# Kernel tuning notes

Hardware: AMD Instinct MI355X
Metric: run time of the kernel (lower is better)

Reference implementation:

```python
import jax, jax.numpy as jnp
import numpy as np

V, E, S, B, T = 100000, 64, 4, 2048, 200
D = 2 * E          # memory_vector_dim
C = E              # controller_units
CIN = 2 * E + D    # controller input: x_t (2E) + prev read (D)
P = 2 * (D + 1) + 2 * D  # (key+beta) for read & write heads + erase + add


def setup_inputs() -> dict:
    key = jax.random.key(0)
    ks = jax.random.split(key, 16)
    g = lambda k, sh, sc=0.05: jax.random.normal(k, sh, dtype=jnp.float32) * sc
    return {
        "item": jax.random.randint(ks[0], (B,), 0, V),
        "cate": jax.random.randint(ks[1], (B,), 0, V),
        "hist_item": jax.random.randint(ks[2], (B, T), 0, V),
        "hist_cate": jax.random.randint(ks[3], (B, T), 0, V),
        "mask": jnp.ones((B, T), jnp.float32),
        "embedding": g(ks[4], (V, E)),
        "gru_Wih": g(ks[5], (3 * C, CIN)),
        "gru_Whh": g(ks[6], (3 * C, C)),
        "gru_bih": jnp.zeros((3 * C,), jnp.float32),
        "gru_bhh": jnp.zeros((3 * C,), jnp.float32),
        "Wp": g(ks[7], (P, C)),
        "bp": jnp.zeros((P,), jnp.float32),
        "Wo": g(ks[8], (E, C + D)),
        "bo": jnp.zeros((E,), jnp.float32),
        "M0": g(ks[9], (S, D), 0.1),
        "fc1_w": g(ks[10], (200, 5 * E)),
        "fc1_b": jnp.zeros((200,), jnp.float32),
        "prelu1_a": jnp.full((1,), 0.25, jnp.float32),
        "fc2_w": g(ks[11], (80, 200)),
        "fc2_b": jnp.zeros((80,), jnp.float32),
        "prelu2_a": jnp.full((1,), 0.25, jnp.float32),
        "fc3_w": g(ks[12], (2, 80)),
        "fc3_b": jnp.zeros((2,), jnp.float32),
    }


def _cos_addr(k, beta, M):
    # content addressing: softmax(beta * cosine_sim(k, M))  k:[B,D] M:[B,S,D]
    kn = k / (jnp.linalg.norm(k, axis=-1, keepdims=True) + 1e-8)
    Mn = M / (jnp.linalg.norm(M, axis=-1, keepdims=True) + 1e-8)
    K = jnp.einsum('bd,bsd->bs', kn, Mn)
    return jax.nn.softmax(beta[:, None] * K, axis=-1)


def _prelu(x, a):
    return jnp.where(x > 0, x, a * x)


def _mimn_rnn(hist_emb, mask, gru_Wih, gru_Whh, gru_bih, gru_bhh, Wp, bp, Wo, bo, M0):
    Bn = hist_emb.shape[0]
    h0 = jnp.zeros((Bn, C), hist_emb.dtype)
    r0 = jnp.zeros((Bn, D), hist_emb.dtype)
    Mi = jnp.broadcast_to(M0[None], (Bn, S, D))

    def step(carry, inp):
        h, M, read = carry
        x_t, m_t = inp                      # x_t [B,2E], m_t [B]
        ctrl_in = jnp.concatenate([x_t, read], axis=-1)
        gi = ctrl_in @ gru_Wih.T + gru_bih
        gh = h @ gru_Whh.T + gru_bhh
        i_r, i_z, i_n = jnp.split(gi, 3, axis=-1)
        h_r, h_z, h_n = jnp.split(gh, 3, axis=-1)
        rg = jax.nn.sigmoid(i_r + h_r)
        zg = jax.nn.sigmoid(i_z + h_z)
        ng = jnp.tanh(i_n + rg * h_n)
        h_new = (1.0 - zg) * ng + zg * h
        # head parameters
        p = h_new @ Wp.T + bp               # [B, P]
        hp_r, hp_w = p[:, :D + 1], p[:, D + 1:2 * (D + 1)]
        erase = jax.nn.sigmoid(p[:, 2 * (D + 1):2 * (D + 1) + D])
        add = jnp.tanh(p[:, -D:])
        k_r, beta_r = jnp.tanh(hp_r[:, :D]), jax.nn.softplus(hp_r[:, D])
        k_w, beta_w = jnp.tanh(hp_w[:, :D]), jax.nn.softplus(hp_w[:, D])
        w_r = _cos_addr(k_r, beta_r, M)
        w_w = _cos_addr(k_w, beta_w, M)
        read_new = jnp.einsum('bs,bsd->bd', w_r, M)
        M_new = M * (1.0 - w_w[..., None] * erase[:, None, :]) + w_w[..., None] * add[:, None, :]
        out = jnp.concatenate([h_new, read_new], axis=-1) @ Wo.T + bo  # [B,E]
        # sequence-length masking (dynamic_rnn semantics)
        v = (m_t > 0)[:, None]
        h = jnp.where(v, h_new, h)
        read = jnp.where(v, read_new, read)
        M = jnp.where(v[..., None], M_new, M)
        out = jnp.where(v, out, jnp.zeros_like(out))
        return (h, M, read), out

    xs = (jnp.swapaxes(hist_emb, 0, 1), jnp.swapaxes(mask, 0, 1))  # [T,B,...]
    _, outs = jax.lax.scan(step, (h0, Mi, r0), xs)
    return jnp.swapaxes(outs, 0, 1)  # [B,T,E]


def reference(item, cate, hist_item, hist_cate, mask, embedding,
              gru_Wih, gru_Whh, gru_bih, gru_bhh, Wp, bp, Wo, bo, M0,
              fc1_w, fc1_b, prelu1_a, fc2_w, fc2_b, prelu2_a, fc3_w, fc3_b):
    item_emb = jnp.concatenate([embedding[item], embedding[cate]], axis=1)      # [B,2E]
    hist_emb = jnp.concatenate([embedding[hist_item], embedding[hist_cate]], axis=2)  # [B,T,2E]
    seq_len = mask.sum(1).astype(jnp.int32)
    outputs = _mimn_rnn(hist_emb, mask, gru_Wih, gru_Whh, gru_bih, gru_bhh, Wp, bp, Wo, bo, M0)
    last_out = jnp.take_along_axis(outputs, (seq_len - 1)[:, None, None], axis=1)[:, 0, :]
    hist_sum = (hist_emb * mask[..., None]).sum(1)                              # [B,2E]
    x = jnp.concatenate([item_emb, hist_sum, last_out], axis=1)                 # [B,5E]
    x = _prelu(x @ fc1_w.T + fc1_b, prelu1_a)
    x = _prelu(x @ fc2_w.T + fc2_b, prelu2_a)
    return x @ fc3_w.T + fc3_b
```

## Files before the change

kernel.cpp:

```cpp
#include <hip/hip_runtime.h>

#define VV 100000
#define BB 2048
#define TT 200
#define GG 192
#define PP 514
#define RPB 8

typedef _Float16 half8 __attribute__((ext_vector_type(8)));
typedef float floatx4 __attribute__((ext_vector_type(4)));
#define MFMA16(a, b, c) __builtin_amdgcn_mfma_f32_16x16x32_f16((a), (b), (c), 0, 0, 0)

__device__ __forceinline__ float fsigm(float x) { return 1.0f / (1.0f + __expf(-x)); }
__device__ __forceinline__ float ftanh(float x) {
    float e = __expf(2.0f * x);
    return 1.0f - 2.0f / (e + 1.0f);
}
__device__ __forceinline__ float fsoftplus(float x) {
    float e = __expf(-fabsf(x));
    return fmaxf(x, 0.0f) + __logf(1.0f + e);
}

#define DPP_ADD(x, ctrl, rmask) \
    ((x) + __int_as_float(__builtin_amdgcn_update_dpp( \
        0, __float_as_int(x), (ctrl), (rmask), 0xf, true)))
__device__ __forceinline__ float wsum64(float x) {
    x = DPP_ADD(x, 0x111, 0xf);
    x = DPP_ADD(x, 0x112, 0xf);
    x = DPP_ADD(x, 0x114, 0xf);
    x = DPP_ADD(x, 0x118, 0xf);
    x = DPP_ADD(x, 0x142, 0xa);
    x = DPP_ADD(x, 0x143, 0xc);
    return __int_as_float(__builtin_amdgcn_readlane(__float_as_int(x), 63));
}
__device__ __forceinline__ float dot4(float4 w, float4 a) {
    return w.x * a.x + w.y * a.y + w.z * a.z + w.w * a.w;
}

__global__ __launch_bounds__(192) void build_tables(
    const float* __restrict__ emb,
    const float* __restrict__ Wih,
    const float* __restrict__ bih,
    float* __restrict__ GIi, float* __restrict__ GIc)
{
    __shared__ float sE[64 * 64];
    int tid = threadIdx.x;
    int v0 = blockIdx.x * 64;
    for (int i = tid; i < 64 * 64; i += 192) {
        int vv = i >> 6, k = i & 63;
        int gv = v0 + vv;
        sE[i] = (gv < VV) ? emb[(size_t)gv * 64 + k] : 0.0f;
    }
    __syncthreads();
    int n = tid;
    float bi = bih[n];
    {
        float4 w[16];
        const float4* wp = (const float4*)(Wih + n * 256);
#pragma unroll
        for (int q = 0; q < 16; ++q) w[q] = wp[q];
        for (int vv = 0; vv < 64; ++vv) {
            int gv = v0 + vv;
            if (gv >= VV) break;
            const float4* e = (const float4*)&sE[vv * 64];
            float acc = bi;
#pragma unroll
            for (int q = 0; q < 16; ++q) acc += dot4(w[q], e[q]);
            GIi[(size_t)gv * GG + n] = acc;
        }
    }
    {
        float4 w[16];
        const float4* wp = (const float4*)(Wih + n * 256 + 64);
#pragma unroll
        for (int q = 0; q < 16; ++q) w[q] = wp[q];
        for (int vv = 0; vv < 64; ++vv) {
            int gv = v0 + vv;
            if (gv >= VV) break;
            const float4* e = (const float4*)&sE[vv * 64];
            float acc = 0.0f;
#pragma unroll
            for (int q = 0; q < 16; ++q) acc += dot4(w[q], e[q]);
            GIc[(size_t)gv * GG + n] = acc;
        }
    }
}

__global__ __launch_bounds__(128) void hist_stats(
    const int* __restrict__ hist_item, const int* __restrict__ hist_cate,
    const float* __restrict__ mask, const float* __restrict__ emb,
    float* __restrict__ hist_sum, int* __restrict__ seqlen)
{
    int b = blockIdx.x, tid = threadIdx.x;
    const int* hidx = (tid < 64) ? hist_item : hist_cate;
    int j = tid & 63;
    float acc = 0.f;
    for (int t = 0; t < TT; ++t) {
        float m = mask[b * TT + t];
        int idx = hidx[b * TT + t];
        acc += m * emb[(size_t)idx * 64 + j];
    }
    hist_sum[(size_t)b * 128 + tid] = acc;
    if (tid < 64) {
        float s = 0.f;
        for (int t = tid; t < TT; t += 64) s += mask[b * TT + t];
        s = wsum64(s);
        if (tid == 0) seqlen[b] = (int)(s + 0.5f);
    }
}

__global__ __attribute__((amdgpu_flat_work_group_size(512, 512))) void mimn_rnn(
    const int* __restrict__ hist_item, const int* __restrict__ hist_cate,
    const float* __restrict__ mask,
    const float* __restrict__ Wih,
    const float* __restrict__ Whh,
    const float* __restrict__ bhh,
    const float* __restrict__ Wp,
    const float* __restrict__ bp,
    const float* __restrict__ Wo,
    const float* __restrict__ bo,
    const float* __restrict__ M0,
    const float* __restrict__ GIi, const float* __restrict__ GIc,
    const int* __restrict__ seqlen,
    float* __restrict__ last_out)
{
    __shared__ __align__(16) float sU[4160];
    __shared__ __align__(16) _Float16 act16[16 * 200];
    __shared__ __align__(16) _Float16 hn16[16 * 72];
    __shared__ __align__(16) float sGI2[2 * RPB * 192];
    __shared__ float sHf[RPB * 64];
    __shared__ float sHnF[RPB * 64];
    __shared__ float sM [RPB * 512];
    __shared__ float sBp[PP];
    __shared__ float sBhh[GG];
    __shared__ float sWpT[2 * 64];
    __shared__ unsigned char sMaskB[RPB * TT];

    const int tid = threadIdx.x;
    const int b0 = blockIdx.x * RPB;
    const int wv = tid >> 6, lane = tid & 63;
    const int nlo = lane & 15, kg = lane >> 4;
    const bool hasN = wv >= 4;

    for (int i = tid; i < 16 * 200; i += 512) act16[i] = (_Float16)0.f;
    for (int i = tid; i < 16 * 72; i += 512) hn16[i] = (_Float16)0.f;
    for (int i = tid; i < RPB * 64; i += 512) { sHf[i] = 0.f; sHnF[i] = 0.f; }
    for (int i = tid; i < RPB * 512; i += 512) sM[i] = M0[i & 511];
    for (int i = tid; i < PP; i += 512) sBp[i] = bp[i];
    if (tid < GG) sBhh[tid] = bhh[tid];
    if (tid < 128) sWpT[tid] = Wp[512 * 64 + tid];
    for (int i = tid; i < RPB * TT; i += 512) {
        int r = i / TT, tt = i - r * TT;
        sMaskB[i] = (mask[(size_t)(b0 + r) * TT + tt] > 0.f) ? 1 : 0;
    }

    half8 WG[6];
    {
        int n = 16 * wv + nlo;
#pragma unroll
        for (int kb = 0; kb < 6; ++kb) {
            half8 f;
#pragma unroll
            for (int j = 0; j < 8; ++j) {
                int k = 32 * kb + 8 * kg + j;
                float w = (k < 128) ? Wih[n * 256 + 128 + k] : Whh[n * 64 + (k - 128)];
                f[j] = (_Float16)w;
            }
            WG[kb] = f;
        }
    }
    half8 WN[6];
    if (hasN) {
        int n = 128 + 16 * (wv - 4) + nlo;
#pragma unroll
        for (int kb = 0; kb < 4; ++kb) {
            half8 f;
#pragma unroll
            for (int j = 0; j < 8; ++j) f[j] = (_Float16)Wih[n * 256 + 128 + 32 * kb + 8 * kg + j];
            WN[kb] = f;
        }
#pragma unroll
        for (int kb = 0; kb < 2; ++kb) {
            half8 f;
#pragma unroll
            for (int j = 0; j < 8; ++j) f[j] = (_Float16)Whh[n * 64 + 32 * kb + 8 * kg + j];
            WN[4 + kb] = f;
        }
    } else {
#pragma unroll
        for (int q = 0; q < 6; ++q) WN[q] = half8{};
    }
    half8 WP[8];
#pragma unroll
    for (int i = 0; i < 4; ++i) {
        int n = 16 * (wv + 8 * i) + nlo;
#pragma unroll
        for (int kb = 0; kb < 2; ++kb) {
            half8 f;
#pragma unroll
            for (int j = 0; j < 8; ++j) f[j] = (_Float16)Wp[n * 64 + 32 * kb + 8 * kg + j];
            WP[2 * i + kb] = f;
        }
    }

    int ts = seqlen[b0 + wv] - 1;
    ts = ts < 0 ? 0 : (ts > TT - 1 ? TT - 1 : ts);
    __syncthreads();

    {
        int ri = hist_item[(size_t)(b0 + wv) * TT];
        int rc = hist_cate[(size_t)(b0 + wv) * TT];
        if (lane < 48) {
            float4 gi = *(const float4*)(GIi + (size_t)ri * GG + lane * 4);
            float4 gc = *(const float4*)(GIc + (size_t)rc * GG + lane * 4);
            *(float4*)&sGI2[wv * 192 + lane * 4] =
                make_float4(gi.x + gc.x, gi.y + gc.y, gi.z + gc.z, gi.w + gc.w);
        }
    }

    for (int t = 0; t < TT; ++t) {
        float4 gi4 = make_float4(0.f, 0.f, 0.f, 0.f);
        float4 gc4 = make_float4(0.f, 0.f, 0.f, 0.f);
        {
            int tn = (t + 1 < TT) ? t + 1 : TT - 1;
            int ri = hist_item[(size_t)(b0 + wv) * TT + tn];
            int rc = hist_cate[(size_t)(b0 + wv) * TT + tn];
            if (lane < 48) {
                gi4 = *(const float4*)(GIi + (size_t)ri * GG + lane * 4);
                gc4 = *(const float4*)(GIc + (size_t)rc * GG + lane * 4);
            }
        }
        {
            const int abase = nlo * 200 + 8 * kg;
            floatx4 accRZ = {0.f, 0.f, 0.f, 0.f};
            floatx4 accI = {0.f, 0.f, 0.f, 0.f};
            floatx4 accH = {0.f, 0.f, 0.f, 0.f};
            half8 a0 = *(const half8*)&act16[abase];
            half8 a1 = *(const half8*)&act16[abase + 32];
            half8 a2 = *(const half8*)&act16[abase + 64];
            accRZ = MFMA16(a0, WG[0], accRZ);
            accRZ = MFMA16(a1, WG[1], accRZ);
            accRZ = MFMA16(a2, WG[2], accRZ);
            if (hasN) {
                accI = MFMA16(a0, WN[0], accI);
                accI = MFMA16(a1, WN[1], accI);
                accI = MFMA16(a2, WN[2], accI);
            }
            a0 = *(const half8*)&act16[abase + 96];
            a1 = *(const half8*)&act16[abase + 128];
            a2 = *(const half8*)&act16[abase + 160];
            accRZ = MFMA16(a0, WG[3], accRZ);
            accRZ = MFMA16(a1, WG[4], accRZ);
            accRZ = MFMA16(a2, WG[5], accRZ);
            if (hasN) {
                accI = MFMA16(a0, WN[3], accI);
                accH = MFMA16(a1, WN[4], accH);
                accH = MFMA16(a2, WN[5], accH);
            }
            if (kg < 2) {
                int n = 16 * wv + nlo;
#pragma unroll
                for (int q = 0; q < 4; ++q) sU[(4 * kg + q) * 132 + n] = accRZ[q];
                if (hasN) {
                    int n64 = 16 * (wv - 4) + nlo;
#pragma unroll
                    for (int q = 0; q < 4; ++q) {
                        sU[1056 + (4 * kg + q) * 68 + n64] = accI[q];
                        sU[1600 + (4 * kg + q) * 68 + n64] = accH[q];
                    }
                }
            }
        }
        __syncthreads();
        {
            const int r = wv;
            const float* gbuf = &sGI2[(t & 1) * 1536 + r * 192];
            float g_r = sU[r * 132 + lane] + gbuf[lane] + sBhh[lane];
            float g_z = sU[r * 132 + 64 + lane] + gbuf[64 + lane] + sBhh[64 + lane];
            float i_n = sU[1056 + r * 68 + lane] + gbuf[128 + lane];
            float h_n = sU[1600 + r * 68 + lane] + sBhh[128 + lane];
            float rg = fsigm(g_r);
            float zg = fsigm(g_z);
            float ng = ftanh(i_n + rg * h_n);
            float h_old = sHf[r * 64 + lane];
            float hn = (1.f - zg) * ng + zg * h_old;
            float hc = sMaskB[r * TT + t] ? hn : h_old;
            sHf[r * 64 + lane] = hc;
            act16[r * 200 + 128 + lane] = (_Float16)hc;
            hn16[r * 72 + lane] = (_Float16)hn;
            sHnF[r * 64 + lane] = hn;
        }
        __syncthreads();
        {
            const int bbase = nlo * 72 + 8 * kg;
            half8 b0f = *(const half8*)&hn16[bbase];
            half8 b1f = *(const half8*)&hn16[bbase + 32];
#pragma unroll
            for (int i = 0; i < 4; ++i) {
                floatx4 acc = {0.f, 0.f, 0.f, 0.f};
                acc = MFMA16(b0f, WP[2 * i], acc);
                acc = MFMA16(b1f, WP[2 * i + 1], acc);
                if (kg < 2) {
                    int n = 16 * (wv + 8 * i) + nlo;
#pragma unroll
                    for (int q = 0; q < 4; ++q) sU[(4 * kg + q) * 520 + n] = acc[q];
                }
            }
        }
        if (tid < 16) {
            int r = tid & 7, j = tid >> 3;
            float acc = 0.f;
#pragma unroll
            for (int k = 0; k < 64; ++k) acc += sHnF[r * 64 + k] * sWpT[j * 64 + k];
            sU[r * 520 + 512 + j] = acc;
        }
        if (lane < 48)
            *(float4*)&sGI2[((t + 1) & 1) * 1536 + wv * 192 + lane * 4] =
                make_float4(gi4.x + gc4.x, gi4.y + gc4.y, gi4.z + gc4.z, gi4.w + gc4.w);
        __syncthreads();
        {
            const int row = wv;
            const int pb = row * 520;
#define PV(n) (sU[pb + (n)] + sBp[(n)])
            float kr1 = ftanh(PV(lane)),       kr2 = ftanh(PV(64 + lane));
            float beta_r = fsoftplus(PV(128));
            float kw1 = ftanh(PV(129 + lane)), kw2 = ftanh(PV(193 + lane));
            float beta_w = fsoftplus(PV(257));
            float er1 = fsigm(PV(258 + lane)), er2 = fsigm(PV(322 + lane));
            float ad1 = ftanh(PV(386 + lane)), ad2 = ftanh(PV(450 + lane));
#undef PV
            float M1[4], M2[4];
#pragma unroll
            for (int s = 0; s < 4; ++s) {
                M1[s] = sM[row * 512 + s * 128 + lane];
                M2[s] = sM[row * 512 + s * 128 + 64 + lane];
            }
            float nkr = sqrtf(wsum64(kr1 * kr1 + kr2 * kr2)) + 1e-8f;
            float nkw = sqrtf(wsum64(kw1 * kw1 + kw2 * kw2)) + 1e-8f;
            float Kr[4], Kw[4];
#pragma unroll
            for (int s = 0; s < 4; ++s) {
                float nM = sqrtf(wsum64(M1[s] * M1[s] + M2[s] * M2[s])) + 1e-8f;
                float dr = wsum64(kr1 * M1[s] + kr2 * M2[s]);
                float dw = wsum64(kw1 * M1[s] + kw2 * M2[s]);
                Kr[s] = dr / (nkr * nM);
                Kw[s] = dw / (nkw * nM);
            }
            float wr_[4], ww_[4];
            {
                float mx = fmaxf(fmaxf(beta_r * Kr[0], beta_r * Kr[1]),
                                 fmaxf(beta_r * Kr[2], beta_r * Kr[3]));
                float sum = 0.f;
#pragma unroll
                for (int s = 0; s < 4; ++s) { wr_[s] = __expf(beta_r * Kr[s] - mx); sum += wr_[s]; }
                float inv = 1.f / sum;
#pragma unroll
                for (int s = 0; s < 4; ++s) wr_[s] *= inv;
            }
            {
                float mx = fmaxf(fmaxf(beta_w * Kw[0], beta_w * Kw[1]),
                                 fmaxf(beta_w * Kw[2], beta_w * Kw[3]));
                float sum = 0.f;
#pragma unroll
                for (int s = 0; s < 4; ++s) { ww_[s] = __expf(beta_w * Kw[s] - mx); sum += ww_[s]; }
                float inv = 1.f / sum;
#pragma unroll
                for (int s = 0; s < 4; ++s) ww_[s] *= inv;
            }
            float rn1 = 0.f, rn2 = 0.f;
#pragma unroll
            for (int s = 0; s < 4; ++s) { rn1 += wr_[s] * M1[s]; rn2 += wr_[s] * M2[s]; }
            bool vld = sMaskB[row * TT + t] != 0;
            if (vld) {
#pragma unroll
                for (int s = 0; s < 4; ++s) {
                    sM[row * 512 + s * 128 + lane]      = M1[s] * (1.f - ww_[s] * er1) + ww_[s] * ad1;
                    sM[row * 512 + s * 128 + 64 + lane] = M2[s] * (1.f - ww_[s] * er2) + ww_[s] * ad2;
                }
                act16[row * 200 + lane]      = (_Float16)rn1;
                act16[row * 200 + 64 + lane] = (_Float16)rn2;
            }
            if (t == ts) {
                float* stash = &sGI2[(t & 1) * 1536 + row * 192];
                stash[lane] = rn1; stash[64 + lane] = rn2;
                __asm__ volatile("s_waitcnt lgkmcnt(0)" ::: "memory");
                float acc = bo[lane];
                const float* wo = Wo + lane * GG;
                for (int k = 0; k < 64; ++k)  acc += sHnF[row * 64 + k] * wo[k];
                for (int k = 0; k < 128; ++k) acc += stash[k] * wo[64 + k];
                if (!vld) acc = 0.f;
                last_out[(size_t)(b0 + row) * 64 + lane] = acc;
            }
        }
        __syncthreads();
    }
}

__global__ __launch_bounds__(128) void final_mlp(
    const int* __restrict__ item, const int* __restrict__ cate,
    const float* __restrict__ emb,
    const float* __restrict__ hist_sum, const float* __restrict__ last_out,
    const float* __restrict__ fc1w, const float* __restrict__ fc1b,
    const float* __restrict__ pa1,
    const float* __restrict__ fc2w, const float* __restrict__ fc2b,
    const float* __restrict__ pa2,
    const float* __restrict__ fc3w, const float* __restrict__ fc3b,
    float* __restrict__ out)
{
    __shared__ float sX[320], sH1[200], sH2[80];
    int b = blockIdx.x, tid = threadIdx.x;
    int it = item[b], ct = cate[b];
    for (int i = tid; i < 320; i += 128) {
        float val;
        if (i < 64)       val = emb[(size_t)it * 64 + i];
        else if (i < 128) val = emb[(size_t)ct * 64 + (i - 64)];
        else if (i < 256) val = hist_sum[(size_t)b * 128 + (i - 128)];
        else              val = last_out[(size_t)b * 64 + (i - 256)];
        sX[i] = val;
    }
    __syncthreads();
    float a1 = pa1[0];
    for (int o = tid; o < 200; o += 128) {
        const float4* w = (const float4*)(fc1w + o * 320);
        float acc = fc1b[o];
#pragma unroll
        for (int q = 0; q < 80; ++q) acc += dot4(w[q], *(const float4*)&sX[q * 4]);
        sH1[o] = acc > 0.f ? acc : a1 * acc;
    }
    __syncthreads();
    float a2 = pa2[0];
    for (int o = tid; o < 80; o += 128) {
        const float4* w = (const float4*)(fc2w + o * 200);
        float acc = fc2b[o];
#pragma unroll
        for (int q = 0; q < 50; ++q) acc += dot4(w[q], *(const float4*)&sH1[q * 4]);
        sH2[o] = acc > 0.f ? acc : a2 * acc;
    }
    __syncthreads();
    if (tid < 2) {
        const float4* w = (const float4*)(fc3w + tid * 80);
        float acc = fc3b[tid];
#pragma unroll
        for (int q = 0; q < 20; ++q) acc += dot4(w[q], *(const float4*)&sH2[q * 4]);
        out[b * 2 + tid] = acc;
    }
}

extern "C" void kernel_launch(void* const* d_in, const int* in_sizes, int n_in,
                              void* d_out, int out_size, void* d_ws, size_t ws_size,
                              hipStream_t stream) {
    (void)in_sizes; (void)n_in; (void)out_size; (void)ws_size;
    const int*   item      = (const int*)d_in[0];
    const int*   cate      = (const int*)d_in[1];
    const int*   hist_item = (const int*)d_in[2];
    const int*   hist_cate = (const int*)d_in[3];
    const float* mask = (const float*)d_in[4];
    const float* emb  = (const float*)d_in[5];
    const float* Wih  = (const float*)d_in[6];
    const float* Whh  = (const float*)d_in[7];
    const float* bih  = (const float*)d_in[8];
    const float* bhh  = (const float*)d_in[9];
    const float* Wp   = (const float*)d_in[10];
    const float* bp   = (const float*)d_in[11];
    const float* Wo   = (const float*)d_in[12];
    const float* bo   = (const float*)d_in[13];
    const float* M0   = (const float*)d_in[14];
    const float* fc1w = (const float*)d_in[15];
    const float* fc1b = (const float*)d_in[16];
    const float* pa1  = (const float*)d_in[17];
    const float* fc2w = (const float*)d_in[18];
    const float* fc2b = (const float*)d_in[19];
    const float* pa2  = (const float*)d_in[20];
    const float* fc3w = (const float*)d_in[21];
    const float* fc3b = (const float*)d_in[22];

    float* GIi = (float*)d_ws;
    float* GIc = GIi + (size_t)VV * GG;
    float* hist_sum = GIc + (size_t)VV * GG;
    float* last_out = hist_sum + (size_t)BB * 128;
    int* seqlen = (int*)(last_out + (size_t)BB * 64);

    build_tables<<<(VV + 63) / 64, 192, 0, stream>>>(emb, Wih, bih, GIi, GIc);
    hist_stats<<<BB, 128, 0, stream>>>(hist_item, hist_cate, mask, emb, hist_sum, seqlen);
    mimn_rnn<<<BB / RPB, 512, 0, stream>>>(hist_item, hist_cate, mask, Wih, Whh, bhh,
                                           Wp, bp, Wo, bo, M0, GIi, GIc, seqlen, last_out);
    final_mlp<<<BB, 128, 0, stream>>>(item, cate, emb, hist_sum, last_out,
                                      fc1w, fc1b, pa1, fc2w, fc2b, pa2, fc3w, fc3b,
                                      (float*)d_out);
}
```

Before: 1.321 ms.

## Keep GRU state, memory and gate inputs in registers; fold biases; lighter barriers

Moves the per-row hidden state, the external memory matrix M and the prefetched gate-input rows out of shared memory into per-lane registers. Biases are preloaded into registers and added when the MFMA results are written, so the per-step bias reads from shared memory go away. __syncthreads is replaced by an LDS-only wait plus s_barrier, and the next-step gather of gate inputs is moved between the GRU stage and the projection stage. This cuts shared-memory traffic and footprint and shortens barrier waits, at the cost of extra registers per thread. The last-step stash now reuses the sU buffer, which relies on sU not being overwritten before the read.

```diff
diff --git a/kernel.cpp b/kernel.cpp
--- a/kernel.cpp
+++ b/kernel.cpp
@@ -10,6 +10,10 @@
 typedef _Float16 half8 __attribute__((ext_vector_type(8)));
 typedef float floatx4 __attribute__((ext_vector_type(4)));
 #define MFMA16(a, b, c) __builtin_amdgcn_mfma_f32_16x16x32_f16((a), (b), (c), 0, 0, 0)
+
+#define BARRIER_LDS() do { \
+    __asm__ volatile("s_waitcnt lgkmcnt(0)" ::: "memory"); \
+    __builtin_amdgcn_s_barrier(); } while (0)
 
 __device__ __forceinline__ float fsigm(float x) { return 1.0f / (1.0f + __expf(-x)); }
 __device__ __forceinline__ float ftanh(float x) {
@@ -127,12 +131,7 @@
     __shared__ __align__(16) float sU[4160];
     __shared__ __align__(16) _Float16 act16[16 * 200];
     __shared__ __align__(16) _Float16 hn16[16 * 72];
-    __shared__ __align__(16) float sGI2[2 * RPB * 192];
-    __shared__ float sHf[RPB * 64];
     __shared__ float sHnF[RPB * 64];
-    __shared__ float sM [RPB * 512];
-    __shared__ float sBp[PP];
-    __shared__ float sBhh[GG];
     __shared__ float sWpT[2 * 64];
     __shared__ unsigned char sMaskB[RPB * TT];
 
@@ -144,16 +143,27 @@
 
     for (int i = tid; i < 16 * 200; i += 512) act16[i] = (_Float16)0.f;
     for (int i = tid; i < 16 * 72; i += 512) hn16[i] = (_Float16)0.f;
-    for (int i = tid; i < RPB * 64; i += 512) { sHf[i] = 0.f; sHnF[i] = 0.f; }
-    for (int i = tid; i < RPB * 512; i += 512) sM[i] = M0[i & 511];
-    for (int i = tid; i < PP; i += 512) sBp[i] = bp[i];
-    if (tid < GG) sBhh[tid] = bhh[tid];
+    for (int i = tid; i < RPB * 64; i += 512) sHnF[i] = 0.f;
     if (tid < 128) sWpT[tid] = Wp[512 * 64 + tid];
     for (int i = tid; i < RPB * TT; i += 512) {
         int r = i / TT, tt = i - r * TT;
         sMaskB[i] = (mask[(size_t)(b0 + r) * TT + tt] > 0.f) ? 1 : 0;
     }
 
+    float hreg = 0.f;
+    float M1[4], M2[4];
+#pragma unroll
+    for (int s = 0; s < 4; ++s) {
+        M1[s] = M0[s * 128 + lane];
+        M2[s] = M0[s * 128 + 64 + lane];
+    }
+    const float bhhRZ = bhh[16 * wv + nlo];
+    const float bhhN  = hasN ? bhh[128 + 16 * (wv - 4) + nlo] : 0.f;
+    float bpP[4];
+#pragma unroll
+    for (int i = 0; i < 4; ++i) bpP[i] = bp[16 * (wv + 8 * i) + nlo];
+    const float bpT = (tid < 16) ? bp[512 + (tid >> 3)] : 0.f;
+
     half8 WG[6];
     {
         int n = 16 * wv + nlo;
@@ -205,31 +215,21 @@
 
     int ts = seqlen[b0 + wv] - 1;
     ts = ts < 0 ? 0 : (ts > TT - 1 ? TT - 1 : ts);
-    __syncthreads();
-
+
+    float giA, giB, giC, gcA, gcB, gcC;
     {
         int ri = hist_item[(size_t)(b0 + wv) * TT];
         int rc = hist_cate[(size_t)(b0 + wv) * TT];
-        if (lane < 48) {
-            float4 gi = *(const float4*)(GIi + (size_t)ri * GG + lane * 4);
-            float4 gc = *(const float4*)(GIc + (size_t)rc * GG + lane * 4);
-            *(float4*)&sGI2[wv * 192 + lane * 4] =
-                make_float4(gi.x + gc.x, gi.y + gc.y, gi.z + gc.z, gi.w + gc.w);
-        }
-    }
+        giA = GIi[(size_t)ri * GG + lane];
+        giB = GIi[(size_t)ri * GG + 64 + lane];
+        giC = GIi[(size_t)ri * GG + 128 + lane];
+        gcA = GIc[(size_t)rc * GG + lane];
+        gcB = GIc[(size_t)rc * GG + 64 + lane];
+        gcC = GIc[(size_t)rc * GG + 128 + lane];
+    }
+    __syncthreads();
 
     for (int t = 0; t < TT; ++t) {
-        float4 gi4 = make_float4(0.f, 0.f, 0.f, 0.f);
-        float4 gc4 = make_float4(0.f, 0.f, 0.f, 0.f);
-        {
-            int tn = (t + 1 < TT) ? t + 1 : TT - 1;
-            int ri = hist_item[(size_t)(b0 + wv) * TT + tn];
-            int rc = hist_cate[(size_t)(b0 + wv) * TT + tn];
-            if (lane < 48) {
-                gi4 = *(const float4*)(GIi + (size_t)ri * GG + lane * 4);
-                gc4 = *(const float4*)(GIc + (size_t)rc * GG + lane * 4);
-            }
-        }
         {
             const int abase = nlo * 200 + 8 * kg;
             floatx4 accRZ = {0.f, 0.f, 0.f, 0.f};
@@ -260,37 +260,48 @@
             if (kg < 2) {
                 int n = 16 * wv + nlo;
 #pragma unroll
-                for (int q = 0; q < 4; ++q) sU[(4 * kg + q) * 132 + n] = accRZ[q];
+                for (int q = 0; q < 4; ++q) sU[(4 * kg + q) * 132 + n] = accRZ[q] + bhhRZ;
                 if (hasN) {
                     int n64 = 16 * (wv - 4) + nlo;
 #pragma unroll
                     for (int q = 0; q < 4; ++q) {
                         sU[1056 + (4 * kg + q) * 68 + n64] = accI[q];
-                        sU[1600 + (4 * kg + q) * 68 + n64] = accH[q];
+                        sU[1600 + (4 * kg + q) * 68 + n64] = accH[q] + bhhN;
                     }
                 }
             }
         }
-        __syncthreads();
+        BARRIER_LDS();
+        bool vld;
         {
             const int r = wv;
-            const float* gbuf = &sGI2[(t & 1) * 1536 + r * 192];
-            float g_r = sU[r * 132 + lane] + gbuf[lane] + sBhh[lane];
-            float g_z = sU[r * 132 + 64 + lane] + gbuf[64 + lane] + sBhh[64 + lane];
-            float i_n = sU[1056 + r * 68 + lane] + gbuf[128 + lane];
-            float h_n = sU[1600 + r * 68 + lane] + sBhh[128 + lane];
+            float g_r = sU[r * 132 + lane] + giA + gcA;
+            float g_z = sU[r * 132 + 64 + lane] + giB + gcB;
+            float i_n = sU[1056 + r * 68 + lane] + giC + gcC;
+            float h_n = sU[1600 + r * 68 + lane];
             float rg = fsigm(g_r);
             float zg = fsigm(g_z);
             float ng = ftanh(i_n + rg * h_n);
-            float h_old = sHf[r * 64 + lane];
-            float hn = (1.f - zg) * ng + zg * h_old;
-            float hc = sMaskB[r * TT + t] ? hn : h_old;
-            sHf[r * 64 + lane] = hc;
+            float hn = (1.f - zg) * ng + zg * hreg;
+            vld = sMaskB[r * TT + t] != 0;
+            float hc = vld ? hn : hreg;
+            hreg = hc;
             act16[r * 200 + 128 + lane] = (_Float16)hc;
             hn16[r * 72 + lane] = (_Float16)hn;
             sHnF[r * 64 + lane] = hn;
         }
-        __syncthreads();
+        {
+            int tn = (t + 1 < TT) ? t + 1 : TT - 1;
+            int ri = hist_item[(size_t)(b0 + wv) * TT + tn];
+            int rc = hist_cate[(size_t)(b0 + wv) * TT + tn];
+            giA = GIi[(size_t)ri * GG + lane];
+            giB = GIi[(size_t)ri * GG + 64 + lane];
+            giC = GIi[(size_t)ri * GG + 128 + lane];
+            gcA = GIc[(size_t)rc * GG + lane];
+            gcB = GIc[(size_t)rc * GG + 64 + lane];
+            gcC = GIc[(size_t)rc * GG + 128 + lane];
+        }
+        BARRIER_LDS();
         {
             const int bbase = nlo * 72 + 8 * kg;
             half8 b0f = *(const half8*)&hn16[bbase];
@@ -303,7 +314,7 @@
                 if (kg < 2) {
                     int n = 16 * (wv + 8 * i) + nlo;
 #pragma unroll
-                    for (int q = 0; q < 4; ++q) sU[(4 * kg + q) * 520 + n] = acc[q];
+                    for (int q = 0; q < 4; ++q) sU[(4 * kg + q) * 520 + n] = acc[q] + bpP[i];
                 }
             }
         }
@@ -312,16 +323,13 @@
             float acc = 0.f;
 #pragma unroll
             for (int k = 0; k < 64; ++k) acc += sHnF[r * 64 + k] * sWpT[j * 64 + k];
-            sU[r * 520 + 512 + j] = acc;
-        }
-        if (lane < 48)
-            *(float4*)&sGI2[((t + 1) & 1) * 1536 + wv * 192 + lane * 4] =
-                make_float4(gi4.x + gc4.x, gi4.y + gc4.y, gi4.z + gc4.z, gi4.w + gc4.w);
-        __syncthreads();
+            sU[r * 520 + 512 + j] = acc + bpT;
+        }
+        BARRIER_LDS();
         {
             const int row = wv;
             const int pb = row * 520;
-#define PV(n) (sU[pb + (n)] + sBp[(n)])
+#define PV(n) (sU[pb + (n)])
             float kr1 = ftanh(PV(lane)),       kr2 = ftanh(PV(64 + lane));
             float beta_r = fsoftplus(PV(128));
             float kw1 = ftanh(PV(129 + lane)), kw2 = ftanh(PV(193 + lane));
@@ -329,12 +337,6 @@
             float er1 = fsigm(PV(258 + lane)), er2 = fsigm(PV(322 + lane));
             float ad1 = ftanh(PV(386 + lane)), ad2 = ftanh(PV(450 + lane));
 #undef PV
-            float M1[4], M2[4];
-#pragma unroll
-            for (int s = 0; s < 4; ++s) {
-                M1[s] = sM[row * 512 + s * 128 + lane];
-                M2[s] = sM[row * 512 + s * 128 + 64 + lane];
-            }
             float nkr = sqrtf(wsum64(kr1 * kr1 + kr2 * kr2)) + 1e-8f;
             float nkw = sqrtf(wsum64(kw1 * kw1 + kw2 * kw2)) + 1e-8f;
             float Kr[4], Kw[4];
@@ -370,18 +372,17 @@
             float rn1 = 0.f, rn2 = 0.f;
 #pragma unroll
             for (int s = 0; s < 4; ++s) { rn1 += wr_[s] * M1[s]; rn2 += wr_[s] * M2[s]; }
-            bool vld = sMaskB[row * TT + t] != 0;
             if (vld) {
 #pragma unroll
                 for (int s = 0; s < 4; ++s) {
-                    sM[row * 512 + s * 128 + lane]      = M1[s] * (1.f - ww_[s] * er1) + ww_[s] * ad1;
-                    sM[row * 512 + s * 128 + 64 + lane] = M2[s] * (1.f - ww_[s] * er2) + ww_[s] * ad2;
+                    M1[s] = M1[s] * (1.f - ww_[s] * er1) + ww_[s] * ad1;
+                    M2[s] = M2[s] * (1.f - ww_[s] * er2) + ww_[s] * ad2;
                 }
                 act16[row * 200 + lane]      = (_Float16)rn1;
                 act16[row * 200 + 64 + lane] = (_Float16)rn2;
             }
             if (t == ts) {
-                float* stash = &sGI2[(t & 1) * 1536 + row * 192];
+                float* stash = &sU[pb];
                 stash[lane] = rn1; stash[64 + lane] = rn2;
                 __asm__ volatile("s_waitcnt lgkmcnt(0)" ::: "memory");
                 float acc = bo[lane];
@@ -392,7 +393,7 @@
                 last_out[(size_t)(b0 + row) * 64 + lane] = acc;
             }
         }
-        __syncthreads();
+        BARRIER_LDS();
     }
 }
 
```

New measurement: 1.270 ms. 3.8% less time.
